# Kernel optimization log

Measured on AMD Instinct MI355X. Metric: run time of the kernel, lower is better.

## Reference

```python
import jax, jax.numpy as jnp
import numpy as np
import math

N, T, D, H = 256, 32, 1024, 1024

def setup_inputs() -> dict:
    key = jax.random.key(0)
    k1, k2, k3, k4, k5 = jax.random.split(key, 5)
    x = jax.random.normal(k1, (N, T, D), dtype=jnp.float32)
    A = jax.random.normal(k2, (N, H, 4, 4), dtype=jnp.float32)
    Wx = jax.random.normal(k3, (D, 4 * H), dtype=jnp.float32) / math.sqrt(D)
    Wh = jax.random.normal(k4, (H, 4 * H), dtype=jnp.float32) / math.sqrt(H)
    Wattn = jax.random.normal(k5, (H, 4 * H), dtype=jnp.float32) / math.sqrt(H)
    b = jnp.zeros((4 * H,), dtype=jnp.float32)
    return {"x": x, "A": A, "Wx": Wx, "Wh": Wh, "Wattn": Wattn, "b": b}

def _forward(x, A, Wx, Wh, Wattn, b):
    Aflat = A.reshape(A.shape[0], A.shape[1], -1)  # (N, H, 16)
    h0 = Aflat.mean(axis=2)  # mean over 4x4 spatial grid -> (N, H)
    c0 = h0
    scale = 1.0 / math.sqrt(Aflat.shape[1])

    def step(carry, xt):
        prev_h, prev_c = carry
        # scaled dot-product attention over 16 spatial locations
        w = jax.nn.softmax(jnp.einsum('nh,nhl->nl', prev_h, Aflat) * scale, axis=-1)  # (N,16)
        attn = jnp.einsum('nhl,nl->nh', Aflat, w)  # (N,H)
        preact = xt @ Wx + prev_h @ Wh + attn @ Wattn + b  # (N,4H)
        ai, af, ao, ag = jnp.split(preact, 4, axis=1)
        i = jax.nn.sigmoid(ai)
        f = jax.nn.sigmoid(af)
        o = jax.nn.sigmoid(ao)
        g = jnp.tanh(ag)
        next_c = f * prev_c + i * g
        next_h = o * jnp.tanh(next_c)
        return (next_h, next_c), next_h

    xT = jnp.swapaxes(x, 0, 1)  # (T, N, D)
    _, hs = jax.lax.scan(step, (h0, c0), xT)
    return jnp.swapaxes(hs, 0, 1)  # (N, T, H)

def reference(x, A, Wx, Wh, Wattn, b):
    return _forward(x, A, Wx, Wh, Wattn, b)
```

## Files before the change

### kernel.cpp

```cpp
#include <hip/hip_runtime.h>

#define N_B 256
#define T_SEQ 32
#define DD 1024
#define HH 1024

typedef short short8 __attribute__((ext_vector_type(8)));
typedef float floatx4 __attribute__((ext_vector_type(4)));
typedef unsigned short ushort_t;

__device__ __align__(16) ushort_t g_Wxt[(size_t)4096 * 1024];
__device__ __align__(16) ushort_t g_W2 [(size_t)4096 * 2048];
__device__ __align__(16) ushort_t g_xb [(size_t)8192 * 1024];
__device__ __align__(16) float    g_px [(size_t)8192 * 4096];
__device__ __align__(16) ushort_t g_Ab [(size_t)N_B * 16384];
__device__ __align__(16) ushort_t g_Hc[2][N_B * 2048];
__device__ __align__(16) float    g_c [N_B * HH];
__device__ __align__(16) float    g_plg[64][N_B][16];

__device__ __forceinline__ float bf2f(ushort_t u){
    union { unsigned int i; float f; } v; v.i = ((unsigned int)u) << 16; return v.f;
}
__device__ __forceinline__ ushort_t f2bf(float f){
    union { unsigned int i; float f; } v; v.f = f;
    unsigned int i = v.i;
    unsigned int r = (i + 0x7FFFu + ((i >> 16) & 1u)) >> 16;
    return (ushort_t)r;
}
__device__ __forceinline__ void gload16(const ushort_t* g, ushort_t* l) {
    __builtin_amdgcn_global_load_lds((const __attribute__((address_space(1))) void*)g,
                                     (__attribute__((address_space(3))) void*)l, 16, 0, 0);
}
__device__ __forceinline__ void unp8(uint4 u, float* f) {
    const ushort_t* s = (const ushort_t*)&u;
    #pragma unroll
    for (int i = 0; i < 8; ++i) f[i] = bf2f(s[i]);
}

__global__ __launch_bounds__(128) void cvt_x(const float* __restrict__ x)
{
    int b = blockIdx.x;
    int n = b >> 5, tt = b & 31;
    int tid = threadIdx.x;
    const float* src = x + (size_t)b * 1024 + tid * 8;
    float4 a = *(const float4*)src;
    float4 c = *(const float4*)(src + 4);
    ushort_t r[8];
    r[0]=f2bf(a.x); r[1]=f2bf(a.y); r[2]=f2bf(a.z); r[3]=f2bf(a.w);
    r[4]=f2bf(c.x); r[5]=f2bf(c.y); r[6]=f2bf(c.z); r[7]=f2bf(c.w);
    *(uint4*)(g_xb + (size_t)(tt * 256 + n) * 1024 + tid * 8) = *(const uint4*)r;
}

__global__ __launch_bounds__(256) void cvt_a(const float* __restrict__ A)
{
    int n = blockIdx.x, tid = threadIdx.x;
    int h0 = tid * 4;
    const float* ap = A + (size_t)n * 16384;
    #pragma unroll
    for (int i = 0; i < 4; ++i) {
        const float* row = ap + (size_t)(h0 + i) * 16;
        ushort_t tmp[16];
        #pragma unroll
        for (int l = 0; l < 16; ++l) tmp[l] = f2bf(row[l]);
        ushort_t* dst = g_Ab + (size_t)n * 16384 + (size_t)(h0 + i) * 16;
        *(uint4*)dst       = *(const uint4*)&tmp[0];
        *(uint4*)(dst + 8) = *(const uint4*)&tmp[8];
    }
}

__global__ __launch_bounds__(256) void prepack_wx(const float* __restrict__ Wx)
{
    __shared__ ushort_t tile[64][66];
    int k0 = blockIdx.x * 64, j0 = blockIdx.y * 64;
    int c = threadIdx.x & 63, r4 = threadIdx.x >> 6;
    for (int rr = 0; rr < 64; rr += 4) {
        int r = rr + r4;
        tile[r][c] = f2bf(Wx[(size_t)(k0 + r) * 4096 + j0 + c]);
    }
    __syncthreads();
    for (int rr = 0; rr < 64; rr += 4) {
        int j = rr + r4;
        g_Wxt[(size_t)(j0 + j) * 1024 + k0 + c] = tile[c][j];
    }
}

__global__ __launch_bounds__(256) void prepack_w2(
    const float* __restrict__ Wh, const float* __restrict__ Wattn)
{
    __shared__ ushort_t tile[64][66];
    int k0 = blockIdx.x * 64, j0 = blockIdx.y * 64;
    const float* src = (k0 < 1024) ? Wh : Wattn;
    int krel = (k0 < 1024) ? k0 : k0 - 1024;
    int c = threadIdx.x & 63, r4 = threadIdx.x >> 6;
    for (int rr = 0; rr < 64; rr += 4) {
        int r = rr + r4;
        tile[r][c] = f2bf(src[(size_t)(krel + r) * 4096 + j0 + c]);
    }
    __syncthreads();
    for (int rr = 0; rr < 64; rr += 4) {
        int j = rr + r4;
        g_W2[(size_t)(j0 + j) * 2048 + k0 + c] = tile[c][j];
    }
}

__global__ __launch_bounds__(256) void init_hc(const float* __restrict__ A)
{
    __shared__ float l1[16 * 257];
    __shared__ float l2[16 * 16];
    __shared__ float lf[16];
    int b = blockIdx.x;
    int n = b >> 2, c = b & 3;
    int tid = threadIdx.x;
    int gid = b * 256 + tid;
    const float* ap = A + ((size_t)gid << 4);
    float a[16];
    *(float4*)(a)      = *(const float4*)(ap);
    *(float4*)(a + 4)  = *(const float4*)(ap + 4);
    *(float4*)(a + 8)  = *(const float4*)(ap + 8);
    *(float4*)(a + 12) = *(const float4*)(ap + 12);
    float s = 0.f;
    #pragma unroll
    for (int l = 0; l < 16; ++l) s += a[l];
    s *= (1.0f / 16.0f);
    g_Hc[0][n * 2048 + (c * 256 + tid)] = f2bf(s);
    g_c[gid] = s;
    #pragma unroll
    for (int l = 0; l < 16; ++l) l1[l * 257 + tid] = s * a[l];
    __syncthreads();
    {
        int l = tid >> 4, seg = tid & 15;
        float s2 = 0.f;
        #pragma unroll
        for (int i = 0; i < 16; ++i) s2 += l1[l * 257 + seg * 16 + i];
        l2[l * 16 + seg] = s2;
    }
    __syncthreads();
    if (tid < 16) {
        float lg = 0.f;
        #pragma unroll
        for (int i = 0; i < 16; ++i) lg += l2[tid * 16 + i];
        lf[tid] = lg;
    }
    __syncthreads();
    int j = tid >> 4, l = tid & 15;
    g_plg[c * 16 + j][n][l] = (j == 0) ? lf[l] : 0.f;
}

__global__ __launch_bounds__(256) void xw_gemm(const float* __restrict__ bias)
{
    __shared__ __align__(16) char smem[33280];
    ushort_t* lA = (ushort_t*)smem;
    ushort_t* lB = (ushort_t*)(smem + 16384);
    float*    lP = (float*)smem;

    int b = blockIdx.x;
    int xcd = b & 7, q = b >> 3;
    int mb = xcd * 8 + (q & 7), jb = q >> 3;
    int m0 = mb * 128, j0 = jb * 128;
    int tid = threadIdx.x, lane = tid & 63, wv = tid >> 6;
    int wm = wv >> 1, wn = wv & 1;
    int lm = lane & 15, quad = lane >> 4;

    int srow = lane >> 3, sseg = lane & 7;
    const ushort_t* gA = g_xb  + (size_t)(m0 + wv * 32 + srow) * 1024 + (sseg ^ srow) * 8;
    const ushort_t* gB = g_Wxt + (size_t)(j0 + wv * 32 + srow) * 1024 + (sseg ^ srow) * 8;

    floatx4 acc[4][4] = {};
    for (int kt = 0; kt < 16; ++kt) {
        __syncthreads();
        #pragma unroll
        for (int i = 0; i < 4; ++i) {
            gload16(gA + (size_t)i * 8 * 1024 + kt * 64, lA + (wv * 32 + i * 8) * 64);
            gload16(gB + (size_t)i * 8 * 1024 + kt * 64, lB + (wv * 32 + i * 8) * 64);
        }
        __syncthreads();
        #pragma unroll
        for (int ks = 0; ks < 2; ++ks) {
            short8 af[4], bf[4];
            #pragma unroll
            for (int i = 0; i < 4; ++i) {
                int row = wm*64 + i*16 + lm;
                af[i] = *(const short8*)(lA + row * 64 + (((ks*4 + quad) ^ (row & 7)) * 8));
            }
            #pragma unroll
            for (int j = 0; j < 4; ++j) {
                int row = wn*64 + j*16 + lm;
                bf[j] = *(const short8*)(lB + row * 64 + (((ks*4 + quad) ^ (row & 7)) * 8));
            }
            #pragma unroll
            for (int i = 0; i < 4; ++i)
                #pragma unroll
                for (int j = 0; j < 4; ++j)
                    acc[i][j] = __builtin_amdgcn_mfma_f32_16x16x32_bf16(af[i], bf[j], acc[i][j], 0, 0, 0);
        }
    }

    #pragma unroll
    for (int ph = 0; ph < 2; ++ph) {
        __syncthreads();
        if (wm == ph) {
            #pragma unroll
            for (int i = 0; i < 4; ++i)
                #pragma unroll
                for (int j = 0; j < 4; ++j)
                    #pragma unroll
                    for (int qq = 0; qq < 4; ++qq)
                        lP[(i*16 + quad*4 + qq) * 130 + wn*64 + j*16 + lm] = acc[i][j][qq];
        }
        __syncthreads();
        int row = tid >> 2, seg = tid & 3;
        const float* src = lP + row * 130 + seg * 32;
        float* dst = g_px + (size_t)(m0 + ph * 64 + row) * 4096 + j0 + seg * 32;
        const float* bb = bias + j0 + seg * 32;
        #pragma unroll
        for (int i = 0; i < 8; ++i) {
            float4 v = *(const float4*)(src + i * 4);
            float4 w = *(const float4*)(bb + i * 4);
            v.x += w.x; v.y += w.y; v.z += w.z; v.w += w.w;
            *(float4*)(dst + i * 4) = v;
        }
    }
}

__global__ __launch_bounds__(256) void attn_step(int t)
{
    ushort_t* Hc = g_Hc[t & 1];
    int n = blockIdx.x, tid = threadIdx.x;
    __shared__ float redm[16 * 17];
    __shared__ float wsh[16];

    {
        int l = tid & 15, j4 = tid >> 4;
        float s = 0.f;
        #pragma unroll
        for (int k = 0; k < 4; ++k) s += g_plg[j4 * 4 + k][n][l];
        redm[j4 * 17 + l] = s;
    }
    __syncthreads();
    if (tid < 16) {
        float lg = 0.f;
        #pragma unroll
        for (int j = 0; j < 16; ++j) lg += redm[j * 17 + tid];
        lg *= 0.03125f;
        float mx = lg;
        mx = fmaxf(mx, __shfl_xor(mx, 1));
        mx = fmaxf(mx, __shfl_xor(mx, 2));
        mx = fmaxf(mx, __shfl_xor(mx, 4));
        mx = fmaxf(mx, __shfl_xor(mx, 8));
        float e = __expf(lg - mx);
        float sm = e;
        sm += __shfl_xor(sm, 1);
        sm += __shfl_xor(sm, 2);
        sm += __shfl_xor(sm, 4);
        sm += __shfl_xor(sm, 8);
        wsh[tid] = e / sm;
    }
    __syncthreads();
    float w[16];
    #pragma unroll
    for (int i = 0; i < 16; ++i) w[i] = wsh[i];

    int h0 = tid * 4;
    const ushort_t* ab = g_Ab + (size_t)n * 16384 + (size_t)h0 * 16;
    ushort_t outp[4];
    #pragma unroll
    for (int i = 0; i < 4; ++i) {
        float av[16];
        unp8(*(const uint4*)(ab + i * 16), av);
        unp8(*(const uint4*)(ab + i * 16 + 8), av + 8);
        float acc = 0.f;
        #pragma unroll
        for (int l = 0; l < 16; ++l) acc += av[l] * w[l];
        outp[i] = f2bf(acc);
    }
    *(uint2*)(Hc + n * 2048 + 1024 + h0) = *(const uint2*)outp;
}

__global__ __launch_bounds__(256, 2) void step_gemm(float* __restrict__ out, int t)
{
    __shared__ __align__(16) char smem[49152];
    ushort_t* lA0 = (ushort_t*)smem;
    ushort_t* lA1 = (ushort_t*)(smem + 8192);
    ushort_t* lB0 = (ushort_t*)(smem + 16384);
    ushort_t* lB1 = (ushort_t*)(smem + 32768);
    float*    lP  = (float*)smem;
    float*    lq  = (float*)smem;

    const ushort_t* Hin  = g_Hc[t & 1];
    ushort_t*       Hout = g_Hc[(t + 1) & 1];

    int b = blockIdx.x;
    int xcd = b & 7, r = b >> 3;
    int jt = xcd * 8 + (r & 7), nt = r >> 3;
    int n0 = nt * 32, hh0 = jt * 16;
    int tid = threadIdx.x, lane = tid & 63, wv = tid >> 6;
    int lm = lane & 15, quad = lane >> 4;

    int srow = lane >> 4, sseg = lane & 15;
    const ushort_t* gA0 = Hin  + (size_t)(n0 + wv * 8 + srow) * 2048;
    const ushort_t* gB0 = g_W2 + (size_t)(wv * 1024 + hh0 + srow) * 2048;

    floatx4 acc[2][4] = {};
    int segk = wv * 4 + quad;

    #pragma unroll
    for (int i = 0; i < 2; ++i) {
        int rlow = (wv * 8 + i * 4 + srow) & 15;
        gload16(gA0 + (size_t)i * 4 * 2048 + (sseg ^ rlow) * 8, lA0 + (wv * 8 + i * 4) * 128);
    }
    #pragma unroll
    for (int i = 0; i < 4; ++i) {
        int rlow = i * 4 + srow;
        gload16(gB0 + (size_t)i * 4 * 2048 + (sseg ^ rlow) * 8, lB0 + (wv * 16 + i * 4) * 128);
    }

    for (int it = 0; it < 16; ++it) {
        ushort_t* cA = (it & 1) ? lA1 : lA0;
        ushort_t* cB = (it & 1) ? lB1 : lB0;
        ushort_t* nA = (it & 1) ? lA0 : lA1;
        ushort_t* nB = (it & 1) ? lB0 : lB1;
        if (it < 15) {
            int kk = (it + 1) * 128;
            #pragma unroll
            for (int i = 0; i < 2; ++i) {
                int rlow = (wv * 8 + i * 4 + srow) & 15;
                gload16(gA0 + (size_t)i * 4 * 2048 + kk + (sseg ^ rlow) * 8,
                        nA + (wv * 8 + i * 4) * 128);
            }
            #pragma unroll
            for (int i = 0; i < 4; ++i) {
                int rlow = i * 4 + srow;
                gload16(gB0 + (size_t)i * 4 * 2048 + kk + (sseg ^ rlow) * 8,
                        nB + (wv * 16 + i * 4) * 128);
            }
            asm volatile("s_waitcnt vmcnt(6)" ::: "memory");
        } else {
            asm volatile("s_waitcnt vmcnt(0)" ::: "memory");
        }
        __builtin_amdgcn_s_barrier();
        short8 af[2], bq[4];
        #pragma unroll
        for (int i = 0; i < 2; ++i)
            af[i] = *(const short8*)(cA + (i * 16 + lm) * 128 + ((segk ^ lm) * 8));
        #pragma unroll
        for (int j = 0; j < 4; ++j)
            bq[j] = *(const short8*)(cB + (j * 16 + lm) * 128 + ((segk ^ lm) * 8));
        #pragma unroll
        for (int i = 0; i < 2; ++i)
            #pragma unroll
            for (int j = 0; j < 4; ++j)
                acc[i][j] = __builtin_amdgcn_mfma_f32_16x16x32_bf16(af[i], bq[j], acc[i][j], 0, 0, 0);
        asm volatile("s_waitcnt lgkmcnt(0)" ::: "memory");
        __builtin_amdgcn_s_barrier();
    }

    float* my = lP + wv * (32 * 68);
    #pragma unroll
    for (int i = 0; i < 2; ++i)
        #pragma unroll
        for (int j = 0; j < 4; ++j)
            #pragma unroll
            for (int q = 0; q < 4; ++q)
                my[(i * 16 + quad * 4 + q) * 68 + j * 16 + lm] = acc[i][j][q];
    __syncthreads();

    float hsave[2];
    #pragma unroll
    for (int e = 0; e < 2; ++e) {
        int idx = tid + e * 256;
        int nl = idx >> 4, hl = idx & 15;
        int base = nl * 68 + hl;
        float s0 = lP[base]      + lP[2176 + base]      + lP[4352 + base]      + lP[6528 + base];
        float s1 = lP[base + 16] + lP[2176 + base + 16] + lP[4352 + base + 16] + lP[6528 + base + 16];
        float s2 = lP[base + 32] + lP[2176 + base + 32] + lP[4352 + base + 32] + lP[6528 + base + 32];
        float s3 = lP[base + 48] + lP[2176 + base + 48] + lP[4352 + base + 48] + lP[6528 + base + 48];
        const float* px = g_px + ((size_t)t * 256 + (n0 + nl)) * 4096 + hh0 + hl;
        float ai  = s0 + px[0];
        float afv = s1 + px[1024];
        float ao  = s2 + px[2048];
        float ag  = s3 + px[3072];
        float iv = 1.f / (1.f + __expf(-ai));
        float fv = 1.f / (1.f + __expf(-afv));
        float ov = 1.f / (1.f + __expf(-ao));
        float gv = tanhf(ag);
        int ng = n0 + nl, hg = hh0 + hl;
        float cold = g_c[ng * 1024 + hg];
        float cnew = fv * cold + iv * gv;
        float hnew = ov * tanhf(cnew);
        g_c[ng * 1024 + hg] = cnew;
        Hout[ng * 2048 + hg] = f2bf(hnew);
        out[(size_t)ng * (T_SEQ * HH) + (size_t)t * HH + hg] = hnew;
        hsave[e] = hnew;
    }

    if (t < 31) {
        __syncthreads();
        #pragma unroll
        for (int e = 0; e < 2; ++e) {
            int idx = tid + e * 256;
            int nl = idx >> 4, hl = idx & 15;
            const ushort_t* ar = g_Ab + (size_t)(n0 + nl) * 16384 + (size_t)(hh0 + hl) * 16;
            float av[16];
            unp8(*(const uint4*)ar, av);
            unp8(*(const uint4*)(ar + 8), av + 8);
            float hv = hsave[e];
            #pragma unroll
            for (int l = 0; l < 16; ++l)
                lq[(nl * 16 + l) * 17 + hl] = hv * av[l];
        }
        __syncthreads();
        #pragma unroll
        for (int e = 0; e < 2; ++e) {
            int idx = tid + e * 256;
            int nl = idx >> 4, l = idx & 15;
            float s = 0.f;
            #pragma unroll
            for (int k = 0; k < 16; ++k) s += lq[(nl * 16 + l) * 17 + k];
            g_plg[jt][n0 + nl][l] = s;
        }
    }
}

extern "C" void kernel_launch(void* const* d_in, const int* in_sizes, int n_in,
                              void* d_out, int out_size, void* d_ws, size_t ws_size,
                              hipStream_t stream) {
    const float* x     = (const float*)d_in[0];
    const float* A     = (const float*)d_in[1];
    const float* Wx    = (const float*)d_in[2];
    const float* Wh    = (const float*)d_in[3];
    const float* Wattn = (const float*)d_in[4];
    const float* bias  = (const float*)d_in[5];
    float* out = (float*)d_out;

    cvt_x<<<8192, 128, 0, stream>>>(x);
    cvt_a<<<256, 256, 0, stream>>>(A);
    prepack_wx<<<dim3(16, 64), 256, 0, stream>>>(Wx);
    prepack_w2<<<dim3(32, 64), 256, 0, stream>>>(Wh, Wattn);
    init_hc<<<1024, 256, 0, stream>>>(A);
    xw_gemm<<<2048, 256, 0, stream>>>(bias);
    for (int t = 0; t < T_SEQ; ++t) {
        attn_step<<<256, 256, 0, stream>>>(t);
        step_gemm<<<512, 256, 0, stream>>>(out, t);
    }
}
```

Measured before the change: 948.8 us.

## Precompute A·Wattn projection so per-step GEMM drops the attention half

Uses associativity: attn @ Wattn = sum_l w_l (A[:,:,l] @ Wattn). A one-time pw_gemm computes P[n,l,:] = A_l @ Wattn in bf16, and each step then only contracts 16 softmax weights against P in the epilogue. The recurrent GEMM K dimension drops from 2048 to 1024. The old attention-vector kernel is replaced by a tiny softmax-only kernel. In exchange this adds a large one-time GEMM, a 128 MB P buffer read every step, and extra bf16 rounding of P.

```diff
diff --git a/kernel.cpp b/kernel.cpp
--- a/kernel.cpp
+++ b/kernel.cpp
@@ -2,21 +2,23 @@
 
 #define N_B 256
 #define T_SEQ 32
-#define DD 1024
-#define HH 1024
 
 typedef short short8 __attribute__((ext_vector_type(8)));
 typedef float floatx4 __attribute__((ext_vector_type(4)));
 typedef unsigned short ushort_t;
 
 __device__ __align__(16) ushort_t g_Wxt[(size_t)4096 * 1024];
-__device__ __align__(16) ushort_t g_W2 [(size_t)4096 * 2048];
+__device__ __align__(16) ushort_t g_Wht[(size_t)4096 * 1024];
+__device__ __align__(16) ushort_t g_Wat[(size_t)4096 * 1024];
 __device__ __align__(16) ushort_t g_xb [(size_t)8192 * 1024];
 __device__ __align__(16) float    g_px [(size_t)8192 * 4096];
 __device__ __align__(16) ushort_t g_Ab [(size_t)N_B * 16384];
-__device__ __align__(16) ushort_t g_Hc[2][N_B * 2048];
-__device__ __align__(16) float    g_c [N_B * HH];
+__device__ __align__(16) ushort_t g_At [(size_t)N_B * 16384];
+__device__ __align__(16) ushort_t g_P  [(size_t)N_B * 4096 * 16];
+__device__ __align__(16) ushort_t g_Hc[2][N_B * 1024];
+__device__ __align__(16) float    g_c [N_B * 1024];
 __device__ __align__(16) float    g_plg[64][N_B][16];
+__device__ __align__(16) float    g_w  [N_B * 16];
 
 __device__ __forceinline__ float bf2f(ushort_t u){
     union { unsigned int i; float f; } v; v.i = ((unsigned int)u) << 16; return v.f;
@@ -56,50 +58,37 @@
     int n = blockIdx.x, tid = threadIdx.x;
     int h0 = tid * 4;
     const float* ap = A + (size_t)n * 16384;
+    ushort_t tmp[4][16];
     #pragma unroll
     for (int i = 0; i < 4; ++i) {
         const float* row = ap + (size_t)(h0 + i) * 16;
-        ushort_t tmp[16];
-        #pragma unroll
-        for (int l = 0; l < 16; ++l) tmp[l] = f2bf(row[l]);
+        #pragma unroll
+        for (int l = 0; l < 16; ++l) tmp[i][l] = f2bf(row[l]);
         ushort_t* dst = g_Ab + (size_t)n * 16384 + (size_t)(h0 + i) * 16;
-        *(uint4*)dst       = *(const uint4*)&tmp[0];
-        *(uint4*)(dst + 8) = *(const uint4*)&tmp[8];
-    }
-}
-
-__global__ __launch_bounds__(256) void prepack_wx(const float* __restrict__ Wx)
+        *(uint4*)dst       = *(const uint4*)&tmp[i][0];
+        *(uint4*)(dst + 8) = *(const uint4*)&tmp[i][8];
+    }
+    #pragma unroll
+    for (int l = 0; l < 16; ++l) {
+        ushort_t pk[4] = { tmp[0][l], tmp[1][l], tmp[2][l], tmp[3][l] };
+        *(uint2*)(g_At + (size_t)n * 16384 + (size_t)l * 1024 + h0) = *(const uint2*)pk;
+    }
+}
+
+__global__ __launch_bounds__(256) void prepack_wT(const float* __restrict__ src, int which)
 {
     __shared__ ushort_t tile[64][66];
+    ushort_t* dst = (which == 0) ? g_Wxt : (which == 1) ? g_Wht : g_Wat;
     int k0 = blockIdx.x * 64, j0 = blockIdx.y * 64;
     int c = threadIdx.x & 63, r4 = threadIdx.x >> 6;
     for (int rr = 0; rr < 64; rr += 4) {
         int r = rr + r4;
-        tile[r][c] = f2bf(Wx[(size_t)(k0 + r) * 4096 + j0 + c]);
+        tile[r][c] = f2bf(src[(size_t)(k0 + r) * 4096 + j0 + c]);
     }
     __syncthreads();
     for (int rr = 0; rr < 64; rr += 4) {
         int j = rr + r4;
-        g_Wxt[(size_t)(j0 + j) * 1024 + k0 + c] = tile[c][j];
-    }
-}
-
-__global__ __launch_bounds__(256) void prepack_w2(
-    const float* __restrict__ Wh, const float* __restrict__ Wattn)
-{
-    __shared__ ushort_t tile[64][66];
-    int k0 = blockIdx.x * 64, j0 = blockIdx.y * 64;
-    const float* src = (k0 < 1024) ? Wh : Wattn;
-    int krel = (k0 < 1024) ? k0 : k0 - 1024;
-    int c = threadIdx.x & 63, r4 = threadIdx.x >> 6;
-    for (int rr = 0; rr < 64; rr += 4) {
-        int r = rr + r4;
-        tile[r][c] = f2bf(src[(size_t)(krel + r) * 4096 + j0 + c]);
-    }
-    __syncthreads();
-    for (int rr = 0; rr < 64; rr += 4) {
-        int j = rr + r4;
-        g_W2[(size_t)(j0 + j) * 2048 + k0 + c] = tile[c][j];
+        dst[(size_t)(j0 + j) * 1024 + k0 + c] = tile[c][j];
     }
 }
 
@@ -122,7 +111,7 @@
     #pragma unroll
     for (int l = 0; l < 16; ++l) s += a[l];
     s *= (1.0f / 16.0f);
-    g_Hc[0][n * 2048 + (c * 256 + tid)] = f2bf(s);
+    g_Hc[0][gid] = f2bf(s);
     g_c[gid] = s;
     #pragma unroll
     for (int l = 0; l < 16; ++l) l1[l * 257 + tid] = s * a[l];
@@ -222,69 +211,103 @@
     }
 }
 
-__global__ __launch_bounds__(256) void attn_step(int t)
-{
-    ushort_t* Hc = g_Hc[t & 1];
+__global__ __launch_bounds__(256) void pw_gemm()
+{
+    __shared__ __align__(16) char smem[32768];
+    ushort_t* lA = (ushort_t*)smem;
+    ushort_t* lB = (ushort_t*)(smem + 16384);
+
+    int b = blockIdx.x;
+    int xcd = b & 7, q = b >> 3;
+    int mb = xcd * 4 + (q & 3), jb = q >> 2;
+    int m0 = mb * 128, j0 = jb * 128;
+    int tid = threadIdx.x, lane = tid & 63, wv = tid >> 6;
+    int wm = wv >> 1, wn = wv & 1;
+    int lm = lane & 15, quad = lane >> 4;
+
+    int srow = lane >> 3, sseg = lane & 7;
+    const ushort_t* gA = g_At  + (size_t)(m0 + wv * 32 + srow) * 1024 + (sseg ^ srow) * 8;
+    const ushort_t* gB = g_Wat + (size_t)(j0 + wv * 32 + srow) * 1024 + (sseg ^ srow) * 8;
+
+    floatx4 acc[4][4] = {};
+    for (int kt = 0; kt < 16; ++kt) {
+        __syncthreads();
+        #pragma unroll
+        for (int i = 0; i < 4; ++i) {
+            gload16(gA + (size_t)i * 8 * 1024 + kt * 64, lA + (wv * 32 + i * 8) * 64);
+            gload16(gB + (size_t)i * 8 * 1024 + kt * 64, lB + (wv * 32 + i * 8) * 64);
+        }
+        __syncthreads();
+        #pragma unroll
+        for (int ks = 0; ks < 2; ++ks) {
+            short8 af[4], bf[4];
+            #pragma unroll
+            for (int i = 0; i < 4; ++i) {
+                int row = wm*64 + i*16 + lm;
+                af[i] = *(const short8*)(lA + row * 64 + (((ks*4 + quad) ^ (row & 7)) * 8));
+            }
+            #pragma unroll
+            for (int j = 0; j < 4; ++j) {
+                int row = wn*64 + j*16 + lm;
+                bf[j] = *(const short8*)(lB + row * 64 + (((ks*4 + quad) ^ (row & 7)) * 8));
+            }
+            #pragma unroll
+            for (int i = 0; i < 4; ++i)
+                #pragma unroll
+                for (int j = 0; j < 4; ++j)
+                    acc[i][j] = __builtin_amdgcn_mfma_f32_16x16x32_bf16(af[i], bf[j], acc[i][j], 0, 0, 0);
+        }
+    }
+
+    int n8 = mb * 8;
+    #pragma unroll
+    for (int i = 0; i < 4; ++i) {
+        #pragma unroll
+        for (int jf = 0; jf < 4; ++jf) {
+            ushort_t pk[4];
+            #pragma unroll
+            for (int q4 = 0; q4 < 4; ++q4) pk[q4] = f2bf(acc[i][jf][q4]);
+            size_t off = ((size_t)(n8 + wm * 4 + i) * 4096
+                          + (j0 + wn * 64 + jf * 16 + lm)) * 16 + quad * 4;
+            *(uint2*)(g_P + off) = *(const uint2*)pk;
+        }
+    }
+}
+
+__global__ __launch_bounds__(64) void attn_w()
+{
     int n = blockIdx.x, tid = threadIdx.x;
-    __shared__ float redm[16 * 17];
-    __shared__ float wsh[16];
-
-    {
-        int l = tid & 15, j4 = tid >> 4;
-        float s = 0.f;
-        #pragma unroll
-        for (int k = 0; k < 4; ++k) s += g_plg[j4 * 4 + k][n][l];
-        redm[j4 * 17 + l] = s;
-    }
-    __syncthreads();
-    if (tid < 16) {
-        float lg = 0.f;
-        #pragma unroll
-        for (int j = 0; j < 16; ++j) lg += redm[j * 17 + tid];
-        lg *= 0.03125f;
-        float mx = lg;
-        mx = fmaxf(mx, __shfl_xor(mx, 1));
-        mx = fmaxf(mx, __shfl_xor(mx, 2));
-        mx = fmaxf(mx, __shfl_xor(mx, 4));
-        mx = fmaxf(mx, __shfl_xor(mx, 8));
-        float e = __expf(lg - mx);
-        float sm = e;
-        sm += __shfl_xor(sm, 1);
-        sm += __shfl_xor(sm, 2);
-        sm += __shfl_xor(sm, 4);
-        sm += __shfl_xor(sm, 8);
-        wsh[tid] = e / sm;
-    }
-    __syncthreads();
-    float w[16];
-    #pragma unroll
-    for (int i = 0; i < 16; ++i) w[i] = wsh[i];
-
-    int h0 = tid * 4;
-    const ushort_t* ab = g_Ab + (size_t)n * 16384 + (size_t)h0 * 16;
-    ushort_t outp[4];
-    #pragma unroll
-    for (int i = 0; i < 4; ++i) {
-        float av[16];
-        unp8(*(const uint4*)(ab + i * 16), av);
-        unp8(*(const uint4*)(ab + i * 16 + 8), av + 8);
-        float acc = 0.f;
-        #pragma unroll
-        for (int l = 0; l < 16; ++l) acc += av[l] * w[l];
-        outp[i] = f2bf(acc);
-    }
-    *(uint2*)(Hc + n * 2048 + 1024 + h0) = *(const uint2*)outp;
+    int l = tid & 15, j4 = tid >> 4;
+    float s = 0.f;
+    #pragma unroll
+    for (int k = 0; k < 16; ++k) s += g_plg[j4 * 16 + k][n][l];
+    s += __shfl_xor(s, 16);
+    s += __shfl_xor(s, 32);
+    float lg = s * 0.03125f;
+    float mx = lg;
+    mx = fmaxf(mx, __shfl_xor(mx, 1));
+    mx = fmaxf(mx, __shfl_xor(mx, 2));
+    mx = fmaxf(mx, __shfl_xor(mx, 4));
+    mx = fmaxf(mx, __shfl_xor(mx, 8));
+    float e = __expf(lg - mx);
+    float sm = e;
+    sm += __shfl_xor(sm, 1);
+    sm += __shfl_xor(sm, 2);
+    sm += __shfl_xor(sm, 4);
+    sm += __shfl_xor(sm, 8);
+    if (tid < 16) g_w[n * 16 + tid] = e / sm;
 }
 
 __global__ __launch_bounds__(256, 2) void step_gemm(float* __restrict__ out, int t)
 {
-    __shared__ __align__(16) char smem[49152];
+    __shared__ __align__(16) char smem[51200];
     ushort_t* lA0 = (ushort_t*)smem;
     ushort_t* lA1 = (ushort_t*)(smem + 8192);
     ushort_t* lB0 = (ushort_t*)(smem + 16384);
     ushort_t* lB1 = (ushort_t*)(smem + 32768);
     float*    lP  = (float*)smem;
     float*    lq  = (float*)smem;
+    float*    lw  = (float*)(smem + 49152);
 
     const ushort_t* Hin  = g_Hc[t & 1];
     ushort_t*       Hout = g_Hc[(t + 1) & 1];
@@ -296,9 +319,12 @@
     int tid = threadIdx.x, lane = tid & 63, wv = tid >> 6;
     int lm = lane & 15, quad = lane >> 4;
 
+    if (tid < 128)
+        *(float4*)(lw + tid * 4) = *(const float4*)(g_w + n0 * 16 + tid * 4);
+
     int srow = lane >> 4, sseg = lane & 15;
-    const ushort_t* gA0 = Hin  + (size_t)(n0 + wv * 8 + srow) * 2048;
-    const ushort_t* gB0 = g_W2 + (size_t)(wv * 1024 + hh0 + srow) * 2048;
+    const ushort_t* gA0 = Hin   + (size_t)(n0 + wv * 8 + srow) * 1024;
+    const ushort_t* gB0 = g_Wht + (size_t)(wv * 1024 + hh0 + srow) * 1024;
 
     floatx4 acc[2][4] = {};
     int segk = wv * 4 + quad;
@@ -306,31 +332,31 @@
     #pragma unroll
     for (int i = 0; i < 2; ++i) {
         int rlow = (wv * 8 + i * 4 + srow) & 15;
-        gload16(gA0 + (size_t)i * 4 * 2048 + (sseg ^ rlow) * 8, lA0 + (wv * 8 + i * 4) * 128);
+        gload16(gA0 + (size_t)i * 4 * 1024 + (sseg ^ rlow) * 8, lA0 + (wv * 8 + i * 4) * 128);
     }
     #pragma unroll
     for (int i = 0; i < 4; ++i) {
         int rlow = i * 4 + srow;
-        gload16(gB0 + (size_t)i * 4 * 2048 + (sseg ^ rlow) * 8, lB0 + (wv * 16 + i * 4) * 128);
-    }
-
-    for (int it = 0; it < 16; ++it) {
+        gload16(gB0 + (size_t)i * 4 * 1024 + (sseg ^ rlow) * 8, lB0 + (wv * 16 + i * 4) * 128);
+    }
+
+    for (int it = 0; it < 8; ++it) {
         ushort_t* cA = (it & 1) ? lA1 : lA0;
         ushort_t* cB = (it & 1) ? lB1 : lB0;
         ushort_t* nA = (it & 1) ? lA0 : lA1;
         ushort_t* nB = (it & 1) ? lB0 : lB1;
-        if (it < 15) {
+        if (it < 7) {
             int kk = (it + 1) * 128;
             #pragma unroll
             for (int i = 0; i < 2; ++i) {
                 int rlow = (wv * 8 + i * 4 + srow) & 15;
-                gload16(gA0 + (size_t)i * 4 * 2048 + kk + (sseg ^ rlow) * 8,
+                gload16(gA0 + (size_t)i * 4 * 1024 + kk + (sseg ^ rlow) * 8,
                         nA + (wv * 8 + i * 4) * 128);
             }
             #pragma unroll
             for (int i = 0; i < 4; ++i) {
                 int rlow = i * 4 + srow;
-                gload16(gB0 + (size_t)i * 4 * 2048 + kk + (sseg ^ rlow) * 8,
+                gload16(gB0 + (size_t)i * 4 * 1024 + kk + (sseg ^ rlow) * 8,
                         nB + (wv * 16 + i * 4) * 128);
             }
             asm volatile("s_waitcnt vmcnt(6)" ::: "memory");
@@ -374,11 +400,28 @@
         float s1 = lP[base + 16] + lP[2176 + base + 16] + lP[4352 + base + 16] + lP[6528 + base + 16];
         float s2 = lP[base + 32] + lP[2176 + base + 32] + lP[4352 + base + 32] + lP[6528 + base + 32];
         float s3 = lP[base + 48] + lP[2176 + base + 48] + lP[4352 + base + 48] + lP[6528 + base + 48];
+        float wreg[16];
+        #pragma unroll
+        for (int k = 0; k < 4; ++k)
+            *(float4*)(wreg + k * 4) = *(const float4*)(lw + nl * 16 + k * 4);
+        const ushort_t* pb = g_P + ((size_t)(n0 + nl) * 4096 + hh0 + hl) * 16;
+        float at[4];
+        #pragma unroll
+        for (int g = 0; g < 4; ++g) {
+            const ushort_t* pg = pb + (size_t)g * 1024 * 16;
+            float pv[16];
+            unp8(*(const uint4*)pg, pv);
+            unp8(*(const uint4*)(pg + 8), pv + 8);
+            float a = 0.f;
+            #pragma unroll
+            for (int l = 0; l < 16; ++l) a += wreg[l] * pv[l];
+            at[g] = a;
+        }
         const float* px = g_px + ((size_t)t * 256 + (n0 + nl)) * 4096 + hh0 + hl;
-        float ai  = s0 + px[0];
-        float afv = s1 + px[1024];
-        float ao  = s2 + px[2048];
-        float ag  = s3 + px[3072];
+        float ai  = s0 + px[0]    + at[0];
+        float afv = s1 + px[1024] + at[1];
+        float ao  = s2 + px[2048] + at[2];
+        float ag  = s3 + px[3072] + at[3];
         float iv = 1.f / (1.f + __expf(-ai));
         float fv = 1.f / (1.f + __expf(-afv));
         float ov = 1.f / (1.f + __expf(-ao));
@@ -388,8 +431,8 @@
         float cnew = fv * cold + iv * gv;
         float hnew = ov * tanhf(cnew);
         g_c[ng * 1024 + hg] = cnew;
-        Hout[ng * 2048 + hg] = f2bf(hnew);
-        out[(size_t)ng * (T_SEQ * HH) + (size_t)t * HH + hg] = hnew;
+        Hout[ng * 1024 + hg] = f2bf(hnew);
+        out[(size_t)ng * (T_SEQ * 1024) + (size_t)t * 1024 + hg] = hnew;
         hsave[e] = hnew;
     }
 
@@ -434,12 +477,14 @@
 
     cvt_x<<<8192, 128, 0, stream>>>(x);
     cvt_a<<<256, 256, 0, stream>>>(A);
-    prepack_wx<<<dim3(16, 64), 256, 0, stream>>>(Wx);
-    prepack_w2<<<dim3(32, 64), 256, 0, stream>>>(Wh, Wattn);
+    prepack_wT<<<dim3(16, 64), 256, 0, stream>>>(Wx, 0);
+    prepack_wT<<<dim3(16, 64), 256, 0, stream>>>(Wh, 1);
+    prepack_wT<<<dim3(16, 64), 256, 0, stream>>>(Wattn, 2);
     init_hc<<<1024, 256, 0, stream>>>(A);
     xw_gemm<<<2048, 256, 0, stream>>>(bias);
+    pw_gemm<<<1024, 256, 0, stream>>>();
     for (int t = 0; t < T_SEQ; ++t) {
-        attn_step<<<256, 256, 0, stream>>>(t);
+        attn_w<<<256, 64, 0, stream>>>();
         step_gemm<<<512, 256, 0, stream>>>(out, t);
     }
 }
```

After: 910.5 us. 4.0% less time.
